# Kernel optimization log

Hardware: AMD Instinct MI355X
Metric: run time of the kernel (lower is better)

Reference implementation:

```python
import jax, jax.numpy as jnp
import numpy as np

T, H, I, R, Z, K = 4096, 1024, 512, 32, 8, 4
E = R + Z
CAP = 768  # per-expert capacity; mean load = T*K/E = 409.6, CAP is ~18 sigma above mean


def setup_inputs() -> dict:
    key = jax.random.key(0)
    k1, k2, k3, k4, k5 = jax.random.split(key, 5)
    hidden_states = jax.random.normal(k1, (T, H), jnp.float32)
    top_k_index = jax.random.randint(k2, (T, K), 0, E).astype(jnp.int64)
    top_k_weights = jax.random.uniform(k3, (T, K), jnp.float32)
    gate_up_proj = jax.random.normal(k4, (E, 2 * I, H), jnp.float32) * 0.02
    down_proj = jax.random.normal(k5, (R, H, I), jnp.float32) * 0.02
    return {
        "hidden_states": hidden_states,
        "top_k_index": top_k_index,
        "top_k_weights": top_k_weights,
        "gate_up_proj": gate_up_proj,
        "down_proj": down_proj,
    }


def reference(hidden_states, top_k_index, top_k_weights, gate_up_proj, down_proj):
    n_tok, h = hidden_states.shape
    k = top_k_index.shape[1]
    n_routed = down_proj.shape[0]
    n_total = gate_up_proj.shape[0]
    A = n_tok * k  # total assignments

    flat_e = top_k_index.reshape(-1).astype(jnp.int32)          # [A]
    flat_t = jnp.repeat(jnp.arange(n_tok, dtype=jnp.int32), k)  # [A]
    flat_w = top_k_weights.reshape(-1)                          # [A]

    # ---- zero experts: weighted identity ----
    zero_w = jnp.sum(jnp.where(top_k_index >= n_routed, top_k_weights, 0.0), axis=1)
    out = hidden_states * zero_w[:, None]

    # ---- routed experts via capacity-buffer grouped GEMM ----
    order = jnp.argsort(flat_e)  # stable sort groups assignments by expert
    se = flat_e[order]
    st = flat_t[order]
    sw = flat_w[order]

    counts = jnp.bincount(flat_e, length=n_total)        # [E]
    starts = jnp.cumsum(counts) - counts                 # exclusive cumsum
    pos = jnp.arange(A, dtype=jnp.int32) - starts[se].astype(jnp.int32)  # slot within expert

    valid = (se < n_routed) & (pos < CAP)
    e_idx = jnp.where(valid, se, 0)
    p_idx = jnp.where(valid, pos, 0)

    xs = jnp.where(valid[:, None], hidden_states[st], 0.0)   # [A,H]
    xbuf = jnp.zeros((n_routed, CAP, h), hidden_states.dtype).at[e_idx, p_idx].add(xs)

    # grouped gated MLP: F.linear(x, W) == x @ W.T with W [out,in]
    gu = jnp.einsum('ech,eoh->eco', xbuf, gate_up_proj[:n_routed])  # [R,CAP,2I]
    gate, up = jnp.split(gu, 2, axis=-1)
    mid = jax.nn.silu(gate) * up                                    # [R,CAP,I]
    ybuf = jnp.einsum('eci,ehi->ech', mid, down_proj)               # [R,CAP,H]

    ya = ybuf[e_idx, p_idx] * jnp.where(valid, sw, 0.0)[:, None]    # [A,H]
    out = out.at[st].add(ya)
    return out
```

## Files before the change

kernel.cpp:

```cpp
#include <hip/hip_runtime.h>
#include <stdint.h>

#define NT 4096
#define HD 1024
#define ID 512
#define RE 32
#define EE 40
#define KT 4
#define CAPACITY 768

typedef __bf16 bf16x8 __attribute__((ext_vector_type(8)));
typedef float f32x4 __attribute__((ext_vector_type(4)));
typedef unsigned int u32x4 __attribute__((ext_vector_type(4)));
typedef unsigned int u32x2 __attribute__((ext_vector_type(2)));
typedef unsigned short u16x4 __attribute__((ext_vector_type(4)));

__device__ __forceinline__ float bf2f(unsigned short u) {
    union { unsigned int i; float f; } v; v.i = ((unsigned int)u) << 16; return v.f;
}
__device__ __forceinline__ unsigned short f2bf(float f) {
    union { float f; unsigned int i; } v; v.f = f;
    unsigned int u = v.i;
    return (unsigned short)((u + 0x7fffu + ((u >> 16) & 1u)) >> 16);
}

__device__ __forceinline__ u32x4 ld8(const void* p, size_t ei, int inF32) {
    if (!inF32) {
        return *(const u32x4*)((const unsigned short*)p + ei);
    } else {
        const float* f = (const float*)p + ei;
        f32x4 a = *(const f32x4*)f;
        f32x4 b = *(const f32x4*)(f + 4);
        u32x4 r;
        r[0] = (unsigned)f2bf(a[0]) | ((unsigned)f2bf(a[1]) << 16);
        r[1] = (unsigned)f2bf(a[2]) | ((unsigned)f2bf(a[3]) << 16);
        r[2] = (unsigned)f2bf(b[0]) | ((unsigned)f2bf(b[1]) << 16);
        r[3] = (unsigned)f2bf(b[2]) | ((unsigned)f2bf(b[3]) << 16);
        return r;
    }
}

typedef __attribute__((address_space(1))) const unsigned int gas_u32;
typedef __attribute__((address_space(3))) unsigned int las_u32;
#define GLL(g, l) __builtin_amdgcn_global_load_lds((gas_u32*)(g), (las_u32*)(l), 16, 0, 0)

__global__ __launch_bounds__(256) void detect_k(const void* __restrict__ X,
                                                const void* __restrict__ idx,
                                                int* __restrict__ flags) {
    __shared__ int sInsane, sOddNZ;
    const int tid = threadIdx.x;
    if (tid == 0) { sInsane = 0; sOddNZ = 0; }
    __syncthreads();
    const unsigned short* xu = (const unsigned short*)X;
    int cnt = 0;
    for (int i = tid; i < 8192; i += 256) {
        int e = (xu[i] >> 7) & 0xFF;
        if (e >= 0x90) cnt++;
    }
    if (cnt) atomicAdd(&sInsane, cnt);
    const int* ip = (const int*)idx;
    int odd = 0;
    for (int i = tid; i < 512; i += 256)
        if ((i & 1) && ip[i] != 0) odd++;
    if (odd) atomicAdd(&sOddNZ, odd);
    __syncthreads();
    if (tid == 0) {
        flags[0] = (sInsane > 64) ? 1 : 0;
        flags[1] = (sOddNZ == 0) ? 1 : 0;
    }
}

__global__ __launch_bounds__(256) void route_k(const int* __restrict__ idx,
                                               const int* __restrict__ flags,
                                               int* __restrict__ cnt,
                                               int* __restrict__ tok,
                                               int* __restrict__ smap) {
    int a = blockIdx.x * 256 + threadIdx.x;
    if (a >= NT * KT) return;
    const int isI64 = flags[1];
    int e = isI64 ? idx[a << 1] : idx[a];
    int s = -1;
    if (e < RE) {
        int slot = atomicAdd(&cnt[e], 1);
        if (slot < CAPACITY) {
            tok[e * CAPACITY + slot] = a >> 2;
            s = slot;
        }
    }
    smap[a] = s;
}

__global__ __launch_bounds__(256) void convert_k(
    const void* __restrict__ X, const void* __restrict__ W1, const void* __restrict__ W2,
    const int* __restrict__ flags,
    unsigned short* __restrict__ Xb, unsigned short* __restrict__ W1b,
    unsigned short* __restrict__ W2b)
{
    const int inF32 = flags[0];
    const size_t gid = (size_t)blockIdx.x * 256 + threadIdx.x;
    const size_t stride = (size_t)gridDim.x * 256;
    const size_t nx = (size_t)NT * HD / 4;
    const size_t n1 = (size_t)RE * 2 * ID * HD / 4;
    const size_t n2 = (size_t)RE * HD * ID / 4;
    if (inF32) {
        for (size_t i = gid; i < nx; i += stride) {
            f32x4 v = ((const f32x4*)X)[i];
            u32x2 r; r[0] = (unsigned)f2bf(v[0]) | ((unsigned)f2bf(v[1]) << 16);
            r[1] = (unsigned)f2bf(v[2]) | ((unsigned)f2bf(v[3]) << 16);
            ((u32x2*)Xb)[i] = r;
        }
        for (size_t i = gid; i < n1; i += stride) {
            f32x4 v = ((const f32x4*)W1)[i];
            u32x2 r; r[0] = (unsigned)f2bf(v[0]) | ((unsigned)f2bf(v[1]) << 16);
            r[1] = (unsigned)f2bf(v[2]) | ((unsigned)f2bf(v[3]) << 16);
            ((u32x2*)W1b)[i] = r;
        }
        for (size_t i = gid; i < n2; i += stride) {
            f32x4 v = ((const f32x4*)W2)[i];
            u32x2 r; r[0] = (unsigned)f2bf(v[0]) | ((unsigned)f2bf(v[1]) << 16);
            r[1] = (unsigned)f2bf(v[2]) | ((unsigned)f2bf(v[3]) << 16);
            ((u32x2*)W2b)[i] = r;
        }
    } else {
        for (size_t i = gid; i < nx; i += stride) ((u32x2*)Xb)[i] = ((const u32x2*)X)[i];
        for (size_t i = gid; i < n1; i += stride) ((u32x2*)W1b)[i] = ((const u32x2*)W1)[i];
        for (size_t i = gid; i < n2; i += stride) ((u32x2*)W2b)[i] = ((const u32x2*)W2)[i];
    }
}

__global__ __launch_bounds__(256, 2) void gemm1n_k(
    const unsigned short* __restrict__ Xb,
    const unsigned short* __restrict__ W1b,
    const int* __restrict__ cnts,
    const int* __restrict__ tok,
    unsigned short* __restrict__ mid)
{
    const int e = blockIdx.z;
    int cnt = cnts[e]; if (cnt > CAPACITY) cnt = CAPACITY;
    const int m0 = blockIdx.x * 128;
    if (m0 >= cnt) return;
    const int n0 = blockIdx.y * 128;

    __shared__ unsigned short Ash[4 * 128 * 8];
    __shared__ unsigned short Bgs[4 * 128 * 8];
    __shared__ unsigned short Bus[4 * 128 * 8];

    const int tid  = threadIdx.x;
    const int lane = tid & 63;
    const int wv   = tid >> 6;
    const int wm   = wv >> 1, wn = wv & 1;
    const int q    = lane >> 4, ln = lane & 15;

    const int r0 = m0 + lane, r1 = m0 + 64 + lane;
    const int t0 = (r0 < cnt) ? tok[e * CAPACITY + r0] : 0;
    const int t1 = (r1 < cnt) ? tok[e * CAPACITY + r1] : 0;
    const unsigned short* gA0 = Xb + (size_t)t0 * HD + wv * 8;
    const unsigned short* gA1 = Xb + (size_t)t1 * HD + wv * 8;
    const unsigned short* gG0 = W1b + ((size_t)e * 1024 + n0 + lane) * HD + wv * 8;
    const unsigned short* gG1 = gG0 + (size_t)64 * HD;
    const unsigned short* gU0 = W1b + ((size_t)e * 1024 + 512 + n0 + lane) * HD + wv * 8;
    const unsigned short* gU1 = gU0 + (size_t)64 * HD;
    unsigned short* lA0 = &Ash[(wv * 128 + 0) * 8];
    unsigned short* lA1 = &Ash[(wv * 128 + 64) * 8];
    unsigned short* lG0 = &Bgs[(wv * 128 + 0) * 8];
    unsigned short* lG1 = &Bgs[(wv * 128 + 64) * 8];
    unsigned short* lU0 = &Bus[(wv * 128 + 0) * 8];
    unsigned short* lU1 = &Bus[(wv * 128 + 64) * 8];

    f32x4 accg[4][4], accu[4][4];
    const f32x4 z4 = {0.f, 0.f, 0.f, 0.f};
    #pragma unroll
    for (int a_ = 0; a_ < 4; a_++)
        #pragma unroll
        for (int b_ = 0; b_ < 4; b_++) { accg[a_][b_] = z4; accu[a_][b_] = z4; }

    #define STAGE1(k0) do { \
        GLL(gA0 + (k0), lA0); GLL(gA1 + (k0), lA1); \
        GLL(gG0 + (k0), lG0); GLL(gG1 + (k0), lG1); \
        GLL(gU0 + (k0), lU0); GLL(gU1 + (k0), lU1); } while (0)

    STAGE1(0);
    for (int k0 = 0; k0 < HD; k0 += 32) {
        __syncthreads();
        bf16x8 af[4], bgf[4], buf2[4];
        #pragma unroll
        for (int mt = 0; mt < 4; mt++)
            af[mt] = *(const bf16x8*)&Ash[(q * 128 + wm * 64 + mt * 16 + ln) * 8];
        #pragma unroll
        for (int nt = 0; nt < 4; nt++) {
            bgf[nt]  = *(const bf16x8*)&Bgs[(q * 128 + wn * 64 + nt * 16 + ln) * 8];
            buf2[nt] = *(const bf16x8*)&Bus[(q * 128 + wn * 64 + nt * 16 + ln) * 8];
        }
        __syncthreads();
        if (k0 + 32 < HD) STAGE1(k0 + 32);
        #pragma unroll
        for (int mt = 0; mt < 4; mt++)
            #pragma unroll
            for (int nt = 0; nt < 4; nt++) {
                accg[mt][nt] = __builtin_amdgcn_mfma_f32_16x16x32_bf16(af[mt], bgf[nt],  accg[mt][nt], 0, 0, 0);
                accu[mt][nt] = __builtin_amdgcn_mfma_f32_16x16x32_bf16(af[mt], buf2[nt], accu[mt][nt], 0, 0, 0);
            }
    }
    #undef STAGE1

    const size_t midBase = (size_t)e * CAPACITY;
    #pragma unroll
    for (int mt = 0; mt < 4; mt++) {
        #pragma unroll
        for (int r = 0; r < 4; r++) {
            int slot = m0 + wm * 64 + mt * 16 + q * 4 + r;
            if (slot < cnt) {
                unsigned short* dst = mid + (midBase + slot) * ID;
                #pragma unroll
                for (int nt = 0; nt < 4; nt++) {
                    int i_col = n0 + wn * 64 + nt * 16 + ln;
                    float gv = accg[mt][nt][r];
                    float uv = accu[mt][nt][r];
                    float sv = gv / (1.f + __expf(-gv));
                    dst[i_col] = f2bf(sv * uv);
                }
            }
        }
    }
}

__global__ __launch_bounds__(256, 2) void gemm2n_k(
    const unsigned short* __restrict__ mid,
    const unsigned short* __restrict__ W2b,
    const int* __restrict__ cnts,
    unsigned short* __restrict__ ybuf)
{
    const int e = blockIdx.z;
    int cnt = cnts[e]; if (cnt > CAPACITY) cnt = CAPACITY;
    const int m0 = blockIdx.x * 128;
    if (m0 >= cnt) return;
    const int n0 = blockIdx.y * 128;

    __shared__ unsigned short Ash[4 * 128 * 8];
    __shared__ unsigned short Bsh[4 * 128 * 8];

    const int tid  = threadIdx.x;
    const int lane = tid & 63;
    const int wv   = tid >> 6;
    const int wm   = wv >> 1, wn = wv & 1;
    const int q    = lane >> 4, ln = lane & 15;

    const unsigned short* gA0 = mid + ((size_t)e * CAPACITY + m0 + lane) * ID + wv * 8;
    const unsigned short* gA1 = gA0 + (size_t)64 * ID;
    const unsigned short* gB0 = W2b + ((size_t)e * HD + n0 + lane) * ID + wv * 8;
    const unsigned short* gB1 = gB0 + (size_t)64 * ID;
    unsigned short* lA0 = &Ash[(wv * 128 + 0) * 8];
    unsigned short* lA1 = &Ash[(wv * 128 + 64) * 8];
    unsigned short* lB0 = &Bsh[(wv * 128 + 0) * 8];
    unsigned short* lB1 = &Bsh[(wv * 128 + 64) * 8];

    f32x4 acc[4][4];
    const f32x4 z4 = {0.f, 0.f, 0.f, 0.f};
    #pragma unroll
    for (int a_ = 0; a_ < 4; a_++)
        #pragma unroll
        for (int b_ = 0; b_ < 4; b_++) acc[a_][b_] = z4;

    #define STAGE2(k0) do { \
        GLL(gA0 + (k0), lA0); GLL(gA1 + (k0), lA1); \
        GLL(gB0 + (k0), lB0); GLL(gB1 + (k0), lB1); } while (0)

    STAGE2(0);
    for (int k0 = 0; k0 < ID; k0 += 32) {
        __syncthreads();
        bf16x8 af[4], bf[4];
        #pragma unroll
        for (int mt = 0; mt < 4; mt++)
            af[mt] = *(const bf16x8*)&Ash[(q * 128 + wm * 64 + mt * 16 + ln) * 8];
        #pragma unroll
        for (int nt = 0; nt < 4; nt++)
            bf[nt] = *(const bf16x8*)&Bsh[(q * 128 + wn * 64 + nt * 16 + ln) * 8];
        __syncthreads();
        if (k0 + 32 < ID) STAGE2(k0 + 32);
        #pragma unroll
        for (int mt = 0; mt < 4; mt++)
            #pragma unroll
            for (int nt = 0; nt < 4; nt++)
                acc[mt][nt] = __builtin_amdgcn_mfma_f32_16x16x32_bf16(af[mt], bf[nt], acc[mt][nt], 0, 0, 0);
    }
    #undef STAGE2

    const size_t yBase = (size_t)e * CAPACITY;
    #pragma unroll
    for (int mt = 0; mt < 4; mt++) {
        #pragma unroll
        for (int r = 0; r < 4; r++) {
            int slot = m0 + wm * 64 + mt * 16 + q * 4 + r;
            if (slot < cnt) {
                unsigned short* dst = ybuf + (yBase + slot) * HD;
                #pragma unroll
                for (int nt = 0; nt < 4; nt++) {
                    int h = n0 + wn * 64 + nt * 16 + ln;
                    dst[h] = f2bf(acc[mt][nt][r]);
                }
            }
        }
    }
}

__global__ __launch_bounds__(256, 2) void gemm1_k(
    const void* __restrict__ X, const void* __restrict__ W1,
    const int* __restrict__ flags, const int* __restrict__ cnts,
    const int* __restrict__ tok, unsigned short* __restrict__ mid)
{
    const int e = blockIdx.z;
    int cnt = cnts[e]; if (cnt > CAPACITY) cnt = CAPACITY;
    const int m0 = blockIdx.x * 128;
    if (m0 >= cnt) return;
    const int n0 = blockIdx.y * 128;
    const int inF32 = flags[0];

    __shared__ unsigned short Ash[4 * 128 * 8];
    __shared__ unsigned short Bgs[4 * 128 * 8];
    __shared__ unsigned short Bus[4 * 128 * 8];

    const int tid  = threadIdx.x;
    const int lane = tid & 63;
    const int wv   = tid >> 6;
    const int wm   = wv >> 1, wn = wv & 1;
    const int q    = lane >> 4, ln = lane & 15;
    const int row = tid & 127;
    const int kcb = tid >> 7;

    const int trow = (m0 + row < cnt) ? tok[e * CAPACITY + m0 + row] : 0;
    const size_t aOff = (size_t)trow * HD;
    const size_t gOff = ((size_t)e * 2 * ID + (n0 + row)) * HD;
    const size_t uOff = ((size_t)e * 2 * ID + (ID + n0 + row)) * HD;

    f32x4 accg[4][4], accu[4][4];
    const f32x4 z4 = {0.f, 0.f, 0.f, 0.f};
    #pragma unroll
    for (int a_ = 0; a_ < 4; a_++)
        #pragma unroll
        for (int b_ = 0; b_ < 4; b_++) { accg[a_][b_] = z4; accu[a_][b_] = z4; }

    u32x4 va[2], vg[2], vu[2];
    #pragma unroll
    for (int i = 0; i < 2; i++) {
        int kc = kcb + 2 * i;
        va[i] = ld8(X,  aOff + kc * 8, inF32);
        vg[i] = ld8(W1, gOff + kc * 8, inF32);
        vu[i] = ld8(W1, uOff + kc * 8, inF32);
    }

    for (int k0 = 0; k0 < HD; k0 += 32) {
        __syncthreads();
        #pragma unroll
        for (int i = 0; i < 2; i++) {
            int kc = kcb + 2 * i;
            *(u32x4*)&Ash[(kc * 128 + row) * 8] = va[i];
            *(u32x4*)&Bgs[(kc * 128 + row) * 8] = vg[i];
            *(u32x4*)&Bus[(kc * 128 + row) * 8] = vu[i];
        }
        __syncthreads();
        if (k0 + 32 < HD) {
            #pragma unroll
            for (int i = 0; i < 2; i++) {
                int kc = kcb + 2 * i;
                va[i] = ld8(X,  aOff + k0 + 32 + kc * 8, inF32);
                vg[i] = ld8(W1, gOff + k0 + 32 + kc * 8, inF32);
                vu[i] = ld8(W1, uOff + k0 + 32 + kc * 8, inF32);
            }
        }
        bf16x8 af[4], bgf[4], buf2[4];
        #pragma unroll
        for (int mt = 0; mt < 4; mt++)
            af[mt] = *(const bf16x8*)&Ash[(q * 128 + wm * 64 + mt * 16 + ln) * 8];
        #pragma unroll
        for (int nt = 0; nt < 4; nt++) {
            bgf[nt]  = *(const bf16x8*)&Bgs[(q * 128 + wn * 64 + nt * 16 + ln) * 8];
            buf2[nt] = *(const bf16x8*)&Bus[(q * 128 + wn * 64 + nt * 16 + ln) * 8];
        }
        #pragma unroll
        for (int mt = 0; mt < 4; mt++)
            #pragma unroll
            for (int nt = 0; nt < 4; nt++) {
                accg[mt][nt] = __builtin_amdgcn_mfma_f32_16x16x32_bf16(af[mt], bgf[nt],  accg[mt][nt], 0, 0, 0);
                accu[mt][nt] = __builtin_amdgcn_mfma_f32_16x16x32_bf16(af[mt], buf2[nt], accu[mt][nt], 0, 0, 0);
            }
    }

    const size_t midBase = (size_t)e * CAPACITY;
    #pragma unroll
    for (int mt = 0; mt < 4; mt++) {
        #pragma unroll
        for (int r = 0; r < 4; r++) {
            int slot = m0 + wm * 64 + mt * 16 + q * 4 + r;
            if (slot < cnt) {
                unsigned short* dst = mid + (midBase + slot) * ID;
                #pragma unroll
                for (int nt = 0; nt < 4; nt++) {
                    int i_col = n0 + wn * 64 + nt * 16 + ln;
                    float gv = accg[mt][nt][r];
                    float uv = accu[mt][nt][r];
                    float sv = gv / (1.f + __expf(-gv));
                    dst[i_col] = f2bf(sv * uv);
                }
            }
        }
    }
}

__global__ __launch_bounds__(256, 2) void gemm2_k(
    const unsigned short* __restrict__ mid, const void* __restrict__ W2,
    const int* __restrict__ flags, const int* __restrict__ cnts,
    unsigned short* __restrict__ ybuf)
{
    const int e = blockIdx.z;
    int cnt = cnts[e]; if (cnt > CAPACITY) cnt = CAPACITY;
    const int m0 = blockIdx.x * 128;
    if (m0 >= cnt) return;
    const int n0 = blockIdx.y * 128;
    const int inF32 = flags[0];

    __shared__ unsigned short Ash[4 * 128 * 8];
    __shared__ unsigned short Bsh[4 * 128 * 8];

    const int tid  = threadIdx.x;
    const int lane = tid & 63;
    const int wv   = tid >> 6;
    const int wm   = wv >> 1, wn = wv & 1;
    const int q    = lane >> 4, ln = lane & 15;
    const int row = tid & 127;
    const int kcb = tid >> 7;

    const unsigned short* aBase = mid + ((size_t)e * CAPACITY + m0 + row) * ID;
    const size_t bOff = ((size_t)e * HD + n0 + row) * ID;

    f32x4 acc[4][4];
    const f32x4 z4 = {0.f, 0.f, 0.f, 0.f};
    #pragma unroll
    for (int a_ = 0; a_ < 4; a_++)
        #pragma unroll
        for (int b_ = 0; b_ < 4; b_++) acc[a_][b_] = z4;

    u32x4 va[2], vb[2];
    #pragma unroll
    for (int i = 0; i < 2; i++) {
        int kc = kcb + 2 * i;
        va[i] = *(const u32x4*)(aBase + kc * 8);
        vb[i] = ld8(W2, bOff + kc * 8, inF32);
    }

    for (int k0 = 0; k0 < ID; k0 += 32) {
        __syncthreads();
        #pragma unroll
        for (int i = 0; i < 2; i++) {
            int kc = kcb + 2 * i;
            *(u32x4*)&Ash[(kc * 128 + row) * 8] = va[i];
            *(u32x4*)&Bsh[(kc * 128 + row) * 8] = vb[i];
        }
        __syncthreads();
        if (k0 + 32 < ID) {
            #pragma unroll
            for (int i = 0; i < 2; i++) {
                int kc = kcb + 2 * i;
                va[i] = *(const u32x4*)(aBase + k0 + 32 + kc * 8);
                vb[i] = ld8(W2, bOff + k0 + 32 + kc * 8, inF32);
            }
        }
        bf16x8 af[4], bf[4];
        #pragma unroll
        for (int mt = 0; mt < 4; mt++)
            af[mt] = *(const bf16x8*)&Ash[(q * 128 + wm * 64 + mt * 16 + ln) * 8];
        #pragma unroll
        for (int nt = 0; nt < 4; nt++)
            bf[nt] = *(const bf16x8*)&Bsh[(q * 128 + wn * 64 + nt * 16 + ln) * 8];
        #pragma unroll
        for (int mt = 0; mt < 4; mt++)
            #pragma unroll
            for (int nt = 0; nt < 4; nt++)
                acc[mt][nt] = __builtin_amdgcn_mfma_f32_16x16x32_bf16(af[mt], bf[nt], acc[mt][nt], 0, 0, 0);
    }

    const size_t yBase = (size_t)e * CAPACITY;
    #pragma unroll
    for (int mt = 0; mt < 4; mt++) {
        #pragma unroll
        for (int r = 0; r < 4; r++) {
            int slot = m0 + wm * 64 + mt * 16 + q * 4 + r;
            if (slot < cnt) {
                unsigned short* dst = ybuf + (yBase + slot) * HD;
                #pragma unroll
                for (int nt = 0; nt < 4; nt++) {
                    int h = n0 + wn * 64 + nt * 16 + ln;
                    dst[h] = f2bf(acc[mt][nt][r]);
                }
            }
        }
    }
}

__global__ __launch_bounds__(256) void gather_k(
    const void* __restrict__ X,
    const int* __restrict__ idx,
    const void* __restrict__ wts,
    const int* __restrict__ flags,
    const int* __restrict__ smap,
    const unsigned short* __restrict__ ybuf,
    float* __restrict__ out)
{
    const int t = blockIdx.x;
    const int tid = threadIdx.x;
    const int inF32 = flags[0];
    __shared__ int se[KT];
    __shared__ float sw[KT];
    __shared__ int ss[KT];
    if (tid < KT) {
        const int isI64 = flags[1];
        int a = t * KT + tid;
        se[tid] = isI64 ? idx[a << 1] : idx[a];
        sw[tid] = inF32 ? ((const float*)wts)[a] : bf2f(((const unsigned short*)wts)[a]);
        ss[tid] = smap[a];
    }
    __syncthreads();

    const int h = tid * 4;
    float x0, x1, x2, x3;
    if (inF32) {
        f32x4 xv = *(const f32x4*)((const float*)X + (size_t)t * HD + h);
        x0 = xv[0]; x1 = xv[1]; x2 = xv[2]; x3 = xv[3];
    } else {
        u16x4 xv = *(const u16x4*)((const unsigned short*)X + (size_t)t * HD + h);
        x0 = bf2f(xv[0]); x1 = bf2f(xv[1]); x2 = bf2f(xv[2]); x3 = bf2f(xv[3]);
    }
    float zw = 0.f;
    #pragma unroll
    for (int k = 0; k < KT; k++)
        if (se[k] >= RE) zw += sw[k];

    float a0 = zw * x0, a1 = zw * x1, a2 = zw * x2, a3 = zw * x3;

    #pragma unroll
    for (int k = 0; k < KT; k++) {
        if (se[k] < RE && ss[k] >= 0) {
            u16x4 yv = *(const u16x4*)&ybuf[((size_t)se[k] * CAPACITY + ss[k]) * HD + h];
            float w = sw[k];
            a0 += w * bf2f(yv[0]);
            a1 += w * bf2f(yv[1]);
            a2 += w * bf2f(yv[2]);
            a3 += w * bf2f(yv[3]);
        }
    }
    f32x4 o = {a0, a1, a2, a3};
    *(f32x4*)&out[(size_t)t * HD + h] = o;
}

extern "C" void kernel_launch(void* const* d_in, const int* in_sizes, int n_in,
                              void* d_out, int out_size, void* d_ws, size_t ws_size,
                              hipStream_t stream) {
    (void)in_sizes; (void)n_in; (void)out_size;
    const void* X   = d_in[0];
    const int*  idx = (const int*)d_in[1];
    const void* wts = d_in[2];
    const void* W1  = d_in[3];
    const void* W2  = d_in[4];
    float* out = (float*)d_out;

    char* ws = (char*)d_ws;
    int* flags = (int*)ws;
    int* cnt   = (int*)(ws + 128);
    int* tok   = (int*)(ws + 256);
    int* smap  = (int*)(ws + 256 + 98304);
    unsigned short* mid = (unsigned short*)(ws + 164224);

    const size_t MIDE = 164224ull + 25165824ull;
    const size_t W2BO = MIDE;
    const size_t XBO  = W2BO + 33554432ull;
    const size_t W1BO = XBO + 8388608ull;
    const size_t NEED = W1BO + 67108864ull;

    hipMemsetAsync(ws, 0, 256, stream);
    detect_k<<<dim3(1), dim3(256), 0, stream>>>(X, idx, flags);
    route_k<<<dim3(64), dim3(256), 0, stream>>>(idx, flags, cnt, tok, smap);

    if (ws_size >= NEED) {
        unsigned short* W2b  = (unsigned short*)(ws + W2BO);
        unsigned short* Xb   = (unsigned short*)(ws + XBO);
        unsigned short* W1b  = (unsigned short*)(ws + W1BO);
        unsigned short* ybuf = (unsigned short*)(ws + W1BO);
        convert_k<<<dim3(2048), dim3(256), 0, stream>>>(X, W1, W2, flags, Xb, W1b, W2b);
        gemm1n_k<<<dim3(6, 4, 32), dim3(256), 0, stream>>>(Xb, W1b, cnt, tok, mid);
        gemm2n_k<<<dim3(6, 8, 32), dim3(256), 0, stream>>>(mid, W2b, cnt, ybuf);
        gather_k<<<dim3(4096), dim3(256), 0, stream>>>(X, idx, wts, flags, smap, ybuf, out);
    } else {
        unsigned short* ybuf = (unsigned short*)(ws + 164224 + 25165824);
        gemm1_k<<<dim3(6, 4, 32), dim3(256), 0, stream>>>(X, W1, flags, cnt, tok, mid);
        gemm2_k<<<dim3(6, 8, 32), dim3(256), 0, stream>>>(mid, W2, flags, cnt, ybuf);
        gather_k<<<dim3(4096), dim3(256), 0, stream>>>(X, idx, wts, flags, smap, ybuf, out);
    }
}
```

Baseline: 493.5 us.

## Fuse combine into down-proj epilogue with atomics and triple-buffer GEMM loads

Routing now records per-slot weights and accumulates zero-expert weights, so the convert pass writes the weighted identity term straight into the output. The down-projection GEMM scatters weighted results into the output with float atomics, which removes the bf16 ybuf round trip and the separate gather kernel. Both GEMMs move from a single shared-memory buffer to a three-stage ring with explicit vmcnt waits, so global loads overlap with MFMA work. In exchange the output becomes order-nondeterministic, atomic contention is added, and shared-memory use grows, which may lower occupancy.

```diff
diff --git a/kernel.cpp b/kernel.cpp
--- a/kernel.cpp
+++ b/kernel.cpp
@@ -71,30 +71,38 @@
 }
 
 __global__ __launch_bounds__(256) void route_k(const int* __restrict__ idx,
+                                               const void* __restrict__ wts,
                                                const int* __restrict__ flags,
                                                int* __restrict__ cnt,
+                                               float* __restrict__ zw,
                                                int* __restrict__ tok,
+                                               float* __restrict__ wslot,
                                                int* __restrict__ smap) {
     int a = blockIdx.x * 256 + threadIdx.x;
     if (a >= NT * KT) return;
     const int isI64 = flags[1];
+    const int inF32 = flags[0];
     int e = isI64 ? idx[a << 1] : idx[a];
+    float w = inF32 ? ((const float*)wts)[a] : bf2f(((const unsigned short*)wts)[a]);
     int s = -1;
     if (e < RE) {
         int slot = atomicAdd(&cnt[e], 1);
         if (slot < CAPACITY) {
             tok[e * CAPACITY + slot] = a >> 2;
+            wslot[e * CAPACITY + slot] = w;
             s = slot;
         }
+    } else {
+        atomicAdd(&zw[a >> 2], w);
     }
     smap[a] = s;
 }
 
 __global__ __launch_bounds__(256) void convert_k(
     const void* __restrict__ X, const void* __restrict__ W1, const void* __restrict__ W2,
-    const int* __restrict__ flags,
+    const int* __restrict__ flags, const float* __restrict__ zw,
     unsigned short* __restrict__ Xb, unsigned short* __restrict__ W1b,
-    unsigned short* __restrict__ W2b)
+    unsigned short* __restrict__ W2b, float* __restrict__ out)
 {
     const int inF32 = flags[0];
     const size_t gid = (size_t)blockIdx.x * 256 + threadIdx.x;
@@ -108,6 +116,9 @@
             u32x2 r; r[0] = (unsigned)f2bf(v[0]) | ((unsigned)f2bf(v[1]) << 16);
             r[1] = (unsigned)f2bf(v[2]) | ((unsigned)f2bf(v[3]) << 16);
             ((u32x2*)Xb)[i] = r;
+            float z = zw[i >> 8];
+            f32x4 o = {z * v[0], z * v[1], z * v[2], z * v[3]};
+            ((f32x4*)out)[i] = o;
         }
         for (size_t i = gid; i < n1; i += stride) {
             f32x4 v = ((const f32x4*)W1)[i];
@@ -122,7 +133,16 @@
             ((u32x2*)W2b)[i] = r;
         }
     } else {
-        for (size_t i = gid; i < nx; i += stride) ((u32x2*)Xb)[i] = ((const u32x2*)X)[i];
+        for (size_t i = gid; i < nx; i += stride) {
+            u32x2 r = ((const u32x2*)X)[i];
+            ((u32x2*)Xb)[i] = r;
+            float z = zw[i >> 8];
+            f32x4 o = {z * bf2f((unsigned short)(r[0] & 0xffffu)),
+                       z * bf2f((unsigned short)(r[0] >> 16)),
+                       z * bf2f((unsigned short)(r[1] & 0xffffu)),
+                       z * bf2f((unsigned short)(r[1] >> 16))};
+            ((f32x4*)out)[i] = o;
+        }
         for (size_t i = gid; i < n1; i += stride) ((u32x2*)W1b)[i] = ((const u32x2*)W1)[i];
         for (size_t i = gid; i < n2; i += stride) ((u32x2*)W2b)[i] = ((const u32x2*)W2)[i];
     }
@@ -141,9 +161,9 @@
     if (m0 >= cnt) return;
     const int n0 = blockIdx.y * 128;
 
-    __shared__ unsigned short Ash[4 * 128 * 8];
-    __shared__ unsigned short Bgs[4 * 128 * 8];
-    __shared__ unsigned short Bus[4 * 128 * 8];
+    __shared__ unsigned short Ash[3 * 4096];
+    __shared__ unsigned short Bgs[3 * 4096];
+    __shared__ unsigned short Bus[3 * 4096];
 
     const int tid  = threadIdx.x;
     const int lane = tid & 63;
@@ -160,12 +180,8 @@
     const unsigned short* gG1 = gG0 + (size_t)64 * HD;
     const unsigned short* gU0 = W1b + ((size_t)e * 1024 + 512 + n0 + lane) * HD + wv * 8;
     const unsigned short* gU1 = gU0 + (size_t)64 * HD;
-    unsigned short* lA0 = &Ash[(wv * 128 + 0) * 8];
-    unsigned short* lA1 = &Ash[(wv * 128 + 64) * 8];
-    unsigned short* lG0 = &Bgs[(wv * 128 + 0) * 8];
-    unsigned short* lG1 = &Bgs[(wv * 128 + 64) * 8];
-    unsigned short* lU0 = &Bus[(wv * 128 + 0) * 8];
-    unsigned short* lU1 = &Bus[(wv * 128 + 64) * 8];
+    const int l0 = (wv * 128 + 0) * 8;
+    const int l1 = (wv * 128 + 64) * 8;
 
     f32x4 accg[4][4], accu[4][4];
     const f32x4 z4 = {0.f, 0.f, 0.f, 0.f};
@@ -174,25 +190,32 @@
         #pragma unroll
         for (int b_ = 0; b_ < 4; b_++) { accg[a_][b_] = z4; accu[a_][b_] = z4; }
 
-    #define STAGE1(k0) do { \
-        GLL(gA0 + (k0), lA0); GLL(gA1 + (k0), lA1); \
-        GLL(gG0 + (k0), lG0); GLL(gG1 + (k0), lG1); \
-        GLL(gU0 + (k0), lU0); GLL(gU1 + (k0), lU1); } while (0)
-
-    STAGE1(0);
-    for (int k0 = 0; k0 < HD; k0 += 32) {
-        __syncthreads();
+    #define STAGE1(k0, b) do { \
+        GLL(gA0 + (k0), &Ash[(b) * 4096 + l0]); GLL(gA1 + (k0), &Ash[(b) * 4096 + l1]); \
+        GLL(gG0 + (k0), &Bgs[(b) * 4096 + l0]); GLL(gG1 + (k0), &Bgs[(b) * 4096 + l1]); \
+        GLL(gU0 + (k0), &Bus[(b) * 4096 + l0]); GLL(gU1 + (k0), &Bus[(b) * 4096 + l1]); } while (0)
+
+    STAGE1(0, 0); STAGE1(32, 1); STAGE1(64, 2);
+
+    int bsel = 0;
+    for (int t = 0; t < 32; ++t) {
+        if (t < 30)       asm volatile("s_waitcnt vmcnt(12)" ::: "memory");
+        else if (t == 30) asm volatile("s_waitcnt vmcnt(6)" ::: "memory");
+        else              asm volatile("s_waitcnt vmcnt(0)" ::: "memory");
+        __builtin_amdgcn_s_barrier();
+        __builtin_amdgcn_sched_barrier(0);
+        const unsigned short* As = &Ash[bsel * 4096];
+        const unsigned short* Gs = &Bgs[bsel * 4096];
+        const unsigned short* Us = &Bus[bsel * 4096];
         bf16x8 af[4], bgf[4], buf2[4];
         #pragma unroll
         for (int mt = 0; mt < 4; mt++)
-            af[mt] = *(const bf16x8*)&Ash[(q * 128 + wm * 64 + mt * 16 + ln) * 8];
+            af[mt] = *(const bf16x8*)&As[(q * 128 + wm * 64 + mt * 16 + ln) * 8];
         #pragma unroll
         for (int nt = 0; nt < 4; nt++) {
-            bgf[nt]  = *(const bf16x8*)&Bgs[(q * 128 + wn * 64 + nt * 16 + ln) * 8];
-            buf2[nt] = *(const bf16x8*)&Bus[(q * 128 + wn * 64 + nt * 16 + ln) * 8];
-        }
-        __syncthreads();
-        if (k0 + 32 < HD) STAGE1(k0 + 32);
+            bgf[nt]  = *(const bf16x8*)&Gs[(q * 128 + wn * 64 + nt * 16 + ln) * 8];
+            buf2[nt] = *(const bf16x8*)&Us[(q * 128 + wn * 64 + nt * 16 + ln) * 8];
+        }
         #pragma unroll
         for (int mt = 0; mt < 4; mt++)
             #pragma unroll
@@ -200,6 +223,12 @@
                 accg[mt][nt] = __builtin_amdgcn_mfma_f32_16x16x32_bf16(af[mt], bgf[nt],  accg[mt][nt], 0, 0, 0);
                 accu[mt][nt] = __builtin_amdgcn_mfma_f32_16x16x32_bf16(af[mt], buf2[nt], accu[mt][nt], 0, 0, 0);
             }
+        asm volatile("s_waitcnt lgkmcnt(0)" ::: "memory");
+        __builtin_amdgcn_sched_barrier(0);
+        __builtin_amdgcn_s_barrier();
+        __builtin_amdgcn_sched_barrier(0);
+        if (t < 29) STAGE1((t + 3) * 32, bsel);
+        bsel++; if (bsel == 3) bsel = 0;
     }
     #undef STAGE1
 
@@ -228,7 +257,9 @@
     const unsigned short* __restrict__ mid,
     const unsigned short* __restrict__ W2b,
     const int* __restrict__ cnts,
-    unsigned short* __restrict__ ybuf)
+    const int* __restrict__ tok,
+    const float* __restrict__ wslot,
+    float* __restrict__ out)
 {
     const int e = blockIdx.z;
     int cnt = cnts[e]; if (cnt > CAPACITY) cnt = CAPACITY;
@@ -236,8 +267,8 @@
     if (m0 >= cnt) return;
     const int n0 = blockIdx.y * 128;
 
-    __shared__ unsigned short Ash[4 * 128 * 8];
-    __shared__ unsigned short Bsh[4 * 128 * 8];
+    __shared__ unsigned short Ash[3 * 4096];
+    __shared__ unsigned short Bsh[3 * 4096];
 
     const int tid  = threadIdx.x;
     const int lane = tid & 63;
@@ -249,10 +280,8 @@
     const unsigned short* gA1 = gA0 + (size_t)64 * ID;
     const unsigned short* gB0 = W2b + ((size_t)e * HD + n0 + lane) * ID + wv * 8;
     const unsigned short* gB1 = gB0 + (size_t)64 * ID;
-    unsigned short* lA0 = &Ash[(wv * 128 + 0) * 8];
-    unsigned short* lA1 = &Ash[(wv * 128 + 64) * 8];
-    unsigned short* lB0 = &Bsh[(wv * 128 + 0) * 8];
-    unsigned short* lB1 = &Bsh[(wv * 128 + 64) * 8];
+    const int l0 = (wv * 128 + 0) * 8;
+    const int l1 = (wv * 128 + 64) * 8;
 
     f32x4 acc[4][4];
     const f32x4 z4 = {0.f, 0.f, 0.f, 0.f};
@@ -261,43 +290,55 @@
         #pragma unroll
         for (int b_ = 0; b_ < 4; b_++) acc[a_][b_] = z4;
 
-    #define STAGE2(k0) do { \
-        GLL(gA0 + (k0), lA0); GLL(gA1 + (k0), lA1); \
-        GLL(gB0 + (k0), lB0); GLL(gB1 + (k0), lB1); } while (0)
-
-    STAGE2(0);
-    for (int k0 = 0; k0 < ID; k0 += 32) {
-        __syncthreads();
+    #define STAGE2(k0, b) do { \
+        GLL(gA0 + (k0), &Ash[(b) * 4096 + l0]); GLL(gA1 + (k0), &Ash[(b) * 4096 + l1]); \
+        GLL(gB0 + (k0), &Bsh[(b) * 4096 + l0]); GLL(gB1 + (k0), &Bsh[(b) * 4096 + l1]); } while (0)
+
+    STAGE2(0, 0); STAGE2(32, 1); STAGE2(64, 2);
+
+    int bsel = 0;
+    for (int t = 0; t < 16; ++t) {
+        if (t < 14)       asm volatile("s_waitcnt vmcnt(8)" ::: "memory");
+        else if (t == 14) asm volatile("s_waitcnt vmcnt(4)" ::: "memory");
+        else              asm volatile("s_waitcnt vmcnt(0)" ::: "memory");
+        __builtin_amdgcn_s_barrier();
+        __builtin_amdgcn_sched_barrier(0);
+        const unsigned short* As = &Ash[bsel * 4096];
+        const unsigned short* Bs = &Bsh[bsel * 4096];
         bf16x8 af[4], bf[4];
         #pragma unroll
         for (int mt = 0; mt < 4; mt++)
-            af[mt] = *(const bf16x8*)&Ash[(q * 128 + wm * 64 + mt * 16 + ln) * 8];
+            af[mt] = *(const bf16x8*)&As[(q * 128 + wm * 64 + mt * 16 + ln) * 8];
         #pragma unroll
         for (int nt = 0; nt < 4; nt++)
-            bf[nt] = *(const bf16x8*)&Bsh[(q * 128 + wn * 64 + nt * 16 + ln) * 8];
-        __syncthreads();
-        if (k0 + 32 < ID) STAGE2(k0 + 32);
+            bf[nt] = *(const bf16x8*)&Bs[(q * 128 + wn * 64 + nt * 16 + ln) * 8];
         #pragma unroll
         for (int mt = 0; mt < 4; mt++)
             #pragma unroll
             for (int nt = 0; nt < 4; nt++)
                 acc[mt][nt] = __builtin_amdgcn_mfma_f32_16x16x32_bf16(af[mt], bf[nt], acc[mt][nt], 0, 0, 0);
+        asm volatile("s_waitcnt lgkmcnt(0)" ::: "memory");
+        __builtin_amdgcn_sched_barrier(0);
+        __builtin_amdgcn_s_barrier();
+        __builtin_amdgcn_sched_barrier(0);
+        if (t < 13) STAGE2((t + 3) * 32, bsel);
+        bsel++; if (bsel == 3) bsel = 0;
     }
     #undef STAGE2
 
-    const size_t yBase = (size_t)e * CAPACITY;
+    const int base = e * CAPACITY;
     #pragma unroll
     for (int mt = 0; mt < 4; mt++) {
         #pragma unroll
         for (int r = 0; r < 4; r++) {
             int slot = m0 + wm * 64 + mt * 16 + q * 4 + r;
             if (slot < cnt) {
-                unsigned short* dst = ybuf + (yBase + slot) * HD;
+                int tt = tok[base + slot];
+                float w = wslot[base + slot];
+                float* dst = out + (size_t)tt * HD + n0 + wn * 64 + ln;
                 #pragma unroll
-                for (int nt = 0; nt < 4; nt++) {
-                    int h = n0 + wn * 64 + nt * 16 + ln;
-                    dst[h] = f2bf(acc[mt][nt][r]);
-                }
+                for (int nt = 0; nt < 4; nt++)
+                    atomicAdd(dst + nt * 16, w * acc[mt][nt][r]);
             }
         }
     }
@@ -563,33 +604,39 @@
     float* out = (float*)d_out;
 
     char* ws = (char*)d_ws;
+    const size_t OFF_CNT  = 128;
+    const size_t OFF_ZW   = 256;
+    const size_t OFF_TOK  = OFF_ZW + 16384;
+    const size_t OFF_WSL  = OFF_TOK + 98304;
+    const size_t OFF_SMAP = OFF_WSL + 98304;
+    const size_t OFF_MID  = OFF_SMAP + 65536;
+    const size_t MID_END  = OFF_MID + 25165824ull;
+    const size_t OFF_W2B  = MID_END;
+    const size_t OFF_XB   = OFF_W2B + 33554432ull;
+    const size_t OFF_W1B  = OFF_XB + 8388608ull;
+    const size_t NEED     = OFF_W1B + 67108864ull;
+
     int* flags = (int*)ws;
-    int* cnt   = (int*)(ws + 128);
-    int* tok   = (int*)(ws + 256);
-    int* smap  = (int*)(ws + 256 + 98304);
-    unsigned short* mid = (unsigned short*)(ws + 164224);
-
-    const size_t MIDE = 164224ull + 25165824ull;
-    const size_t W2BO = MIDE;
-    const size_t XBO  = W2BO + 33554432ull;
-    const size_t W1BO = XBO + 8388608ull;
-    const size_t NEED = W1BO + 67108864ull;
-
-    hipMemsetAsync(ws, 0, 256, stream);
+    int* cnt   = (int*)(ws + OFF_CNT);
+    float* zw  = (float*)(ws + OFF_ZW);
+    int* tok   = (int*)(ws + OFF_TOK);
+    float* wsl = (float*)(ws + OFF_WSL);
+    int* smap  = (int*)(ws + OFF_SMAP);
+    unsigned short* mid = (unsigned short*)(ws + OFF_MID);
+
+    hipMemsetAsync(ws, 0, OFF_ZW + 16384, stream);
     detect_k<<<dim3(1), dim3(256), 0, stream>>>(X, idx, flags);
-    route_k<<<dim3(64), dim3(256), 0, stream>>>(idx, flags, cnt, tok, smap);
+    route_k<<<dim3(64), dim3(256), 0, stream>>>(idx, wts, flags, cnt, zw, tok, wsl, smap);
 
     if (ws_size >= NEED) {
-        unsigned short* W2b  = (unsigned short*)(ws + W2BO);
-        unsigned short* Xb   = (unsigned short*)(ws + XBO);
-        unsigned short* W1b  = (unsigned short*)(ws + W1BO);
-        unsigned short* ybuf = (unsigned short*)(ws + W1BO);
-        convert_k<<<dim3(2048), dim3(256), 0, stream>>>(X, W1, W2, flags, Xb, W1b, W2b);
+        unsigned short* W2b = (unsigned short*)(ws + OFF_W2B);
+        unsigned short* Xb  = (unsigned short*)(ws + OFF_XB);
+        unsigned short* W1b = (unsigned short*)(ws + OFF_W1B);
+        convert_k<<<dim3(2048), dim3(256), 0, stream>>>(X, W1, W2, flags, zw, Xb, W1b, W2b, out);
         gemm1n_k<<<dim3(6, 4, 32), dim3(256), 0, stream>>>(Xb, W1b, cnt, tok, mid);
-        gemm2n_k<<<dim3(6, 8, 32), dim3(256), 0, stream>>>(mid, W2b, cnt, ybuf);
-        gather_k<<<dim3(4096), dim3(256), 0, stream>>>(X, idx, wts, flags, smap, ybuf, out);
+        gemm2n_k<<<dim3(6, 8, 32), dim3(256), 0, stream>>>(mid, W2b, cnt, tok, wsl, out);
     } else {
-        unsigned short* ybuf = (unsigned short*)(ws + 164224 + 25165824);
+        unsigned short* ybuf = (unsigned short*)(ws + MID_END);
         gemm1_k<<<dim3(6, 4, 32), dim3(256), 0, stream>>>(X, W1, flags, cnt, tok, mid);
         gemm2_k<<<dim3(6, 8, 32), dim3(256), 0, stream>>>(mid, W2, flags, cnt, ybuf);
         gather_k<<<dim3(4096), dim3(256), 0, stream>>>(X, idx, wts, flags, smap, ybuf, out);
```

After: 521.5 us. +5.7%, slower.
